# Kernel tuning notes

Measured on AMD Instinct MI355X. Metric: run time of the kernel, lower is better.

## Reference

```python
import jax, jax.numpy as jnp
import numpy as np

NUM_USERS = 100000
NUM_ITEMS = 50000
N_NODES = NUM_USERS + NUM_ITEMS
EMB = 64
N_EDGES = 2000000
NUM_LAYERS = 3


def setup_inputs() -> dict:
    key = jax.random.key(0)
    ks = jax.random.split(key, 16)
    inp = {
        "edge_index": jax.random.randint(ks[0], (2, N_EDGES), 0, N_NODES, dtype=jnp.int64 if jax.config.jax_enable_x64 else jnp.int32),
        "user_features": jax.random.normal(ks[1], (NUM_USERS, 15), dtype=jnp.float32),
        "user_color_indices": jax.random.randint(ks[2], (NUM_USERS,), 0, 22),
        "user_size_indices": jax.random.randint(ks[3], (NUM_USERS,), 0, 18),
        "item_features": jax.random.normal(ks[4], (NUM_ITEMS, 17), dtype=jnp.float32),
        "user_emb_w": jax.random.normal(ks[5], (NUM_USERS, EMB), dtype=jnp.float32) * 0.01,
        "item_emb_w": jax.random.normal(ks[6], (NUM_ITEMS, EMB), dtype=jnp.float32) * 0.01,
        "user_numeric_W": jax.random.normal(ks[7], (EMB, 12), dtype=jnp.float32) * 0.1,
        "user_numeric_b": jnp.zeros((EMB,), dtype=jnp.float32),
        "user_vector_W": jax.random.normal(ks[8], (EMB, 3), dtype=jnp.float32) * 0.1,
        "user_vector_b": jnp.zeros((EMB,), dtype=jnp.float32),
        "color_emb_w": jax.random.normal(ks[9], (22, EMB), dtype=jnp.float32) * 0.1,
        "size_emb_w": jax.random.normal(ks[10], (18, EMB), dtype=jnp.float32) * 0.1,
        "item_numeric_W": jax.random.normal(ks[11], (EMB, 5), dtype=jnp.float32) * 0.1,
        "item_numeric_b": jnp.zeros((EMB,), dtype=jnp.float32),
        "item_vector_W": jax.random.normal(ks[12], (EMB, 12), dtype=jnp.float32) * 0.1,
        "item_vector_b": jnp.zeros((EMB,), dtype=jnp.float32),
    }
    return inp


def _lightgcn_conv(x, row, col, norm):
    # gather x at source (row), scale by per-edge norm, scatter-add at target (col)
    msg = norm[:, None] * x[row]                      # [E, d]
    return jax.ops.segment_sum(msg, col, num_segments=N_NODES)


def reference(edge_index, user_features, user_color_indices, user_size_indices,
              item_features, user_emb_w, item_emb_w,
              user_numeric_W, user_numeric_b, user_vector_W, user_vector_b,
              color_emb_w, size_emb_w,
              item_numeric_W, item_numeric_b, item_vector_W, item_vector_b):
    # multimodal feature fusion
    user_emb = (user_emb_w
                + user_features[:, :12] @ user_numeric_W.T + user_numeric_b
                + user_features[:, 12:15] @ user_vector_W.T + user_vector_b
                + color_emb_w[user_color_indices]
                + size_emb_w[user_size_indices])
    item_emb = (item_emb_w
                + item_features[:, :5] @ item_numeric_W.T + item_numeric_b
                + item_features[:, 5:] @ item_vector_W.T + item_vector_b)
    x = jnp.concatenate([user_emb, item_emb], axis=0)  # [N, d]

    row, col = edge_index[0], edge_index[1]
    # symmetric-normalization coefficients (degree over targets, as in source)
    deg = jax.ops.segment_sum(jnp.ones_like(col, dtype=x.dtype), col, num_segments=N_NODES)
    deg_inv_sqrt = jnp.where(deg > 0, jax.lax.rsqrt(jnp.maximum(deg, 1.0)), 0.0)
    norm = deg_inv_sqrt[row] * deg_inv_sqrt[col]       # [E]

    acc = x
    total = x
    for _ in range(NUM_LAYERS):
        acc = _lightgcn_conv(acc, row, col, norm)      # dropout in eval mode = identity
        total = total + acc
    final = total / (NUM_LAYERS + 1)

    return final[:NUM_USERS], final[NUM_USERS:]
```

## Files before the change

### kernel.cpp

```cpp
#include <hip/hip_runtime.h>

#define EMB 64
#define NBMAX 512
#define BCAP 8192
#define BSTRIDE 12288
#define CHUNK 4096


__device__ __forceinline__ unsigned short f2bf(float f) {
    union { float f; unsigned u; } c; c.f = f;
    unsigned r = c.u + 0x7fffu + ((c.u >> 16) & 1u);
    return (unsigned short)(r >> 16);
}
__device__ __forceinline__ float bflo(unsigned u) {
    union { unsigned u; float f; } c; c.u = u << 16; return c.f;
}
__device__ __forceinline__ float bfhi(unsigned u) {
    union { unsigned u; float f; } c; c.u = u & 0xffff0000u; return c.f;
}
__device__ __forceinline__ unsigned pack2(float a, float b) {
    return (unsigned)f2bf(a) | ((unsigned)f2bf(b) << 16);
}


__global__ void init_kernel(unsigned* __restrict__ p, int nz,
                            unsigned* __restrict__ dummyA,
                            unsigned* __restrict__ dummyB) {
    int i = blockIdx.x * blockDim.x + threadIdx.x;
    if (i < nz) p[i] = 0u;
    if (blockIdx.x == 0) {
        int t = threadIdx.x;
        if (t < 32) dummyA[t] = 0u;
        else if (t < 64) dummyB[t - 32] = 0u;
    }
}


__global__ void fuse_users_kernel(const float* __restrict__ feat,
                                  const int* __restrict__ cidx,
                                  const int* __restrict__ sidx,
                                  const float* __restrict__ emb_w,
                                  const float* __restrict__ Wn,
                                  const float* __restrict__ bn,
                                  const float* __restrict__ Wv,
                                  const float* __restrict__ bv,
                                  const float* __restrict__ color_w,
                                  const float* __restrict__ size_w,
                                  const float* __restrict__ dis,
                                  unsigned short* __restrict__ totB,
                                  unsigned short* __restrict__ y0,
                                  int U) {
    int t = blockIdx.x * blockDim.x + threadIdx.x;
    int u = t >> 6, d = t & 63;
    if (u >= U) return;
    const float* f = feat + (size_t)u * 15;
    float acc = emb_w[(size_t)u * EMB + d] + bn[d] + bv[d];
#pragma unroll
    for (int k = 0; k < 12; ++k) acc = fmaf(f[k], Wn[d * 12 + k], acc);
#pragma unroll
    for (int k = 0; k < 3; ++k) acc = fmaf(f[12 + k], Wv[d * 3 + k], acc);
    acc += color_w[(size_t)cidx[u] * EMB + d];
    acc += size_w[(size_t)sidx[u] * EMB + d];
    size_t o = (size_t)u * EMB + d;
    totB[o] = f2bf(acc);
    y0[o] = f2bf(acc * dis[u]);
}

__global__ void fuse_items_kernel(const float* __restrict__ feat,
                                  const float* __restrict__ emb_w,
                                  const float* __restrict__ Wn,
                                  const float* __restrict__ bn,
                                  const float* __restrict__ Wv,
                                  const float* __restrict__ bv,
                                  const float* __restrict__ dis,
                                  unsigned short* __restrict__ totB,
                                  unsigned short* __restrict__ y0,
                                  int I, int U) {
    int t = blockIdx.x * blockDim.x + threadIdx.x;
    int i = t >> 6, d = t & 63;
    if (i >= I) return;
    const float* f = feat + (size_t)i * 17;
    float acc = emb_w[(size_t)i * EMB + d] + bn[d] + bv[d];
#pragma unroll
    for (int k = 0; k < 5; ++k) acc = fmaf(f[k], Wn[d * 5 + k], acc);
#pragma unroll
    for (int k = 0; k < 12; ++k) acc = fmaf(f[5 + k], Wv[d * 12 + k], acc);
    int n = U + i;
    size_t o = (size_t)n * EMB + d;
    totB[o] = f2bf(acc);
    y0[o] = f2bf(acc * dis[n]);
}


__global__ __launch_bounds__(512) void partition_kernel(
        const int* __restrict__ row, const int* __restrict__ col,
        unsigned* __restrict__ bcursor, unsigned* __restrict__ bucketbuf,
        int E, int NB) {
    __shared__ unsigned h[NBMAX];
    __shared__ unsigned wbase[NBMAX];
    const int t = threadIdx.x;
    const long chunk = (long)blockIdx.x * CHUNK;

    for (int i = t; i < NB; i += 512) h[i] = 0u;
    __syncthreads();
    for (int it = 0; it < CHUNK / 2048; ++it) {
        long e = chunk + (long)it * 2048 + t * 4;
        if (e + 3 < E) {
            uint4 c4 = *reinterpret_cast<const uint4*>(&col[e]);
            atomicAdd(&h[c4.x >> 9], 1u); atomicAdd(&h[c4.y >> 9], 1u);
            atomicAdd(&h[c4.z >> 9], 1u); atomicAdd(&h[c4.w >> 9], 1u);
        } else {
            for (int k = 0; k < 4; ++k) {
                long ek = e + k;
                if (ek < E) atomicAdd(&h[((unsigned)col[ek]) >> 9], 1u);
            }
        }
    }
    __syncthreads();
    for (int i = t; i < NB; i += 512) {
        unsigned c = h[i];
        wbase[i] = c ? atomicAdd(&bcursor[i], c) : 0u;
    }
    __syncthreads();
    for (int i = t; i < NB; i += 512) h[i] = 0u;
    __syncthreads();
    for (int it = 0; it < CHUNK / 2048; ++it) {
        long e = chunk + (long)it * 2048 + t * 4;
        if (e + 3 < E) {
            uint4 c4 = *reinterpret_cast<const uint4*>(&col[e]);
            uint4 r4 = *reinterpret_cast<const uint4*>(&row[e]);
            unsigned cs[4] = {c4.x, c4.y, c4.z, c4.w};
            unsigned rs[4] = {r4.x, r4.y, r4.z, r4.w};
#pragma unroll
            for (int k = 0; k < 4; ++k) {
                unsigned b = cs[k] >> 9;
                unsigned pos = wbase[b] + atomicAdd(&h[b], 1u);
                if (pos < BCAP)
                    bucketbuf[(size_t)b * BCAP + pos] = (rs[k] << 9) | (cs[k] & 511u);
            }
        } else {
            for (int k = 0; k < 4; ++k) {
                long ek = e + k;
                if (ek < E) {
                    unsigned c = (unsigned)col[ek];
                    unsigned b = c >> 9;
                    unsigned pos = wbase[b] + atomicAdd(&h[b], 1u);
                    if (pos < BCAP)
                        bucketbuf[(size_t)b * BCAP + pos] =
                            (((unsigned)row[ek]) << 9) | (c & 511u);
                }
            }
        }
    }
}


__global__ __launch_bounds__(512) void bucket_csr_kernel(
        const unsigned* __restrict__ bcursor,
        const unsigned* __restrict__ bucketbuf,
        uint4* __restrict__ meta,
        float* __restrict__ dis, unsigned* __restrict__ srcidx,
        unsigned* __restrict__ order,
        int N, int NB) {
    const int b = blockIdx.x;
    const int t = threadIdx.x;
    __shared__ unsigned hist[512];
    __shared__ unsigned ps[512];
    __shared__ unsigned cls[64];
    __shared__ unsigned clsB[64];

    const unsigned base = (unsigned)b * BSTRIDE;
    unsigned cntb = bcursor[b];
    if (cntb > BCAP) cntb = BCAP;

    hist[t] = 0u;
    if (t < 64) cls[t] = 0u;
    __syncthreads();
    const unsigned* buf = bucketbuf + (size_t)b * BCAP;
    for (unsigned j = t; j < cntb; j += 512) atomicAdd(&hist[buf[j] & 511u], 1u);
    __syncthreads();

    unsigned h0 = hist[t];
    unsigned c0p = (h0 + 7u) & ~7u;
    ps[t] = c0p;
    __syncthreads();
    for (int off = 1; off < 512; off <<= 1) {
        unsigned y = (t >= off) ? ps[t - off] : 0u;
        __syncthreads();
        ps[t] += y;
        __syncthreads();
    }
    unsigned beg0 = base + ps[t] - c0p;

    int n0 = (b << 9) + t;
    unsigned c = min(c0p >> 3, 63u), lpos = 0;
    if (n0 < N) {
        float dv = h0 ? rsqrtf((float)h0) : 0.f;
        meta[n0] = make_uint4(beg0, beg0 + c0p, __float_as_uint(dv), 0u);
        dis[n0] = dv;
        lpos = atomicAdd(&cls[c], 1u);
        for (unsigned k = h0; k < c0p; ++k) srcidx[beg0 + k] = ((unsigned)N) << 5;
    }
    __syncthreads();
    if (t == 0) {
        unsigned run = 0;
        for (int i = 0; i < 64; ++i) { unsigned v = cls[i]; clsB[i] = run; run += v; }
    }
    __syncthreads();
    if (n0 < N) order[(b << 9) + clsB[c] + lpos] = (unsigned)n0;

    hist[t] = beg0;
    __syncthreads();
    for (unsigned j = t; j < cntb; j += 512) {
        unsigned p = buf[j];
        unsigned pos = atomicAdd(&hist[p & 511u], 1u);
        srcidx[pos] = (p >> 9) << 5;
    }
}


__global__ __launch_bounds__(256) void gather_propagate_kernel(
        const unsigned* __restrict__ order, const uint4* __restrict__ meta,
        const unsigned* __restrict__ src,
        const unsigned* __restrict__ srcidx,
        unsigned* __restrict__ ynext,
        unsigned* __restrict__ totB,
        float4* __restrict__ outF,
        int N, int mode) {
    int lane = threadIdx.x & 63;
    int slot = blockIdx.x * 8 + ((threadIdx.x >> 6) << 1) + (lane >> 5);
    bool active = slot < N;
    int n = active ? (int)order[slot] : 0;
    uint4 md = active ? meta[n] : make_uint4(0u, 0u, 0u, 0u);
    unsigned beg = md.x, endp = md.y;
    float dn = __uint_as_float(md.z);
    unsigned q = (unsigned)((lane >> 4) & 1);
    unsigned m2 = (unsigned)(lane & 15) * 2u;
    size_t o = (size_t)n * 32 + m2;
    uint2 tv = *reinterpret_cast<const uint2*>(&totB[o]);
    float s0 = 0.f, s1 = 0.f, s2 = 0.f, s3 = 0.f;
    float t0 = 0.f, t1 = 0.f, t2 = 0.f, t3 = 0.f;
    unsigned j = beg;
    for (; j + 16 <= endp; j += 16) {
        uint4 iv0 = *reinterpret_cast<const uint4*>(&srcidx[j + 4u * q]);
        uint4 iv1 = *reinterpret_cast<const uint4*>(&srcidx[j + 8u + 4u * q]);
        uint2 ua = *reinterpret_cast<const uint2*>(&src[iv0.x + m2]);
        uint2 ub = *reinterpret_cast<const uint2*>(&src[iv0.y + m2]);
        uint2 uc = *reinterpret_cast<const uint2*>(&src[iv0.z + m2]);
        uint2 ud = *reinterpret_cast<const uint2*>(&src[iv0.w + m2]);
        uint2 ue = *reinterpret_cast<const uint2*>(&src[iv1.x + m2]);
        uint2 uf = *reinterpret_cast<const uint2*>(&src[iv1.y + m2]);
        uint2 ug = *reinterpret_cast<const uint2*>(&src[iv1.z + m2]);
        uint2 uh = *reinterpret_cast<const uint2*>(&src[iv1.w + m2]);
        s0 += (bflo(ua.x) + bflo(ub.x)) + (bflo(uc.x) + bflo(ud.x));
        s1 += (bfhi(ua.x) + bfhi(ub.x)) + (bfhi(uc.x) + bfhi(ud.x));
        s2 += (bflo(ua.y) + bflo(ub.y)) + (bflo(uc.y) + bflo(ud.y));
        s3 += (bfhi(ua.y) + bfhi(ub.y)) + (bfhi(uc.y) + bfhi(ud.y));
        t0 += (bflo(ue.x) + bflo(uf.x)) + (bflo(ug.x) + bflo(uh.x));
        t1 += (bfhi(ue.x) + bfhi(uf.x)) + (bfhi(ug.x) + bfhi(uh.x));
        t2 += (bflo(ue.y) + bflo(uf.y)) + (bflo(ug.y) + bflo(uh.y));
        t3 += (bfhi(ue.y) + bfhi(uf.y)) + (bfhi(ug.y) + bfhi(uh.y));
    }
    if (j < endp) {
        uint4 iv = *reinterpret_cast<const uint4*>(&srcidx[j + 4u * q]);
        uint2 ua = *reinterpret_cast<const uint2*>(&src[iv.x + m2]);
        uint2 ub = *reinterpret_cast<const uint2*>(&src[iv.y + m2]);
        uint2 uc = *reinterpret_cast<const uint2*>(&src[iv.z + m2]);
        uint2 ud = *reinterpret_cast<const uint2*>(&src[iv.w + m2]);
        s0 += (bflo(ua.x) + bflo(ub.x)) + (bflo(uc.x) + bflo(ud.x));
        s1 += (bfhi(ua.x) + bfhi(ub.x)) + (bfhi(uc.x) + bfhi(ud.x));
        s2 += (bflo(ua.y) + bflo(ub.y)) + (bflo(uc.y) + bflo(ud.y));
        s3 += (bfhi(ua.y) + bfhi(ub.y)) + (bfhi(uc.y) + bfhi(ud.y));
    }
    s0 += t0; s1 += t1; s2 += t2; s3 += t3;
    s0 += __shfl_xor(s0, 16);
    s1 += __shfl_xor(s1, 16);
    s2 += __shfl_xor(s2, 16);
    s3 += __shfl_xor(s3, 16);
    if (active && (lane & 31) < 16) {
        float a0 = dn * s0, a1 = dn * s1, a2 = dn * s2, a3 = dn * s3;
        float b0 = bflo(tv.x) + a0, b1 = bfhi(tv.x) + a1;
        float b2 = bflo(tv.y) + a2, b3 = bfhi(tv.y) + a3;
        if (mode == 0) {
            uint2 nv;
            nv.x = pack2(b0, b1);
            nv.y = pack2(b2, b3);
            *reinterpret_cast<uint2*>(&totB[o]) = nv;
            uint2 pk;
            pk.x = pack2(dn * a0, dn * a1);
            pk.y = pack2(dn * a2, dn * a3);
            *reinterpret_cast<uint2*>(&ynext[(size_t)n * 32 + m2]) = pk;
        } else {
            outF[(size_t)n * 16 + (m2 >> 1)] =
                make_float4(b0 * 0.25f, b1 * 0.25f, b2 * 0.25f, b3 * 0.25f);
        }
    }
}


extern "C" void kernel_launch(void* const* d_in, const int* in_sizes, int n_in,
                              void* d_out, int out_size, void* d_ws, size_t ws_size,
                              hipStream_t stream) {
    const int*   edge       = (const int*)d_in[0];
    const float* user_feat  = (const float*)d_in[1];
    const int*   cidx       = (const int*)d_in[2];
    const int*   sidx       = (const int*)d_in[3];
    const float* item_feat  = (const float*)d_in[4];
    const float* user_emb_w = (const float*)d_in[5];
    const float* item_emb_w = (const float*)d_in[6];
    const float* uWn        = (const float*)d_in[7];
    const float* ubn        = (const float*)d_in[8];
    const float* uWv        = (const float*)d_in[9];
    const float* ubv        = (const float*)d_in[10];
    const float* color_w    = (const float*)d_in[11];
    const float* size_w     = (const float*)d_in[12];
    const float* iWn        = (const float*)d_in[13];
    const float* ibn        = (const float*)d_in[14];
    const float* iWv        = (const float*)d_in[15];
    const float* ibv        = (const float*)d_in[16];

    const int E = in_sizes[0] / 2;
    const int U = in_sizes[5] / EMB;
    const int I = in_sizes[6] / EMB;
    const int N = U + I;
    const int NB = (N + 511) >> 9;

    const int* row = edge;
    const int* col = edge + E;

    unsigned short* yA      = (unsigned short*)d_ws;
    unsigned short* yB      = yA + (size_t)(N + 1) * EMB;
    unsigned*       bucketbuf = (unsigned*)yB;
    unsigned short* totB    = yB + (size_t)(N + 1) * EMB;
    unsigned*       srcidx  = (unsigned*)(totB + (size_t)N * EMB);
    uint4*          meta    = (uint4*)(srcidx + (size_t)NB * BSTRIDE);
    float*          dis     = (float*)(meta + N);
    unsigned*       bcursor = (unsigned*)(dis + N);
    unsigned*       order   = bcursor + NB;

    const int TB = 256;

    init_kernel<<<(NB + TB - 1) / TB, TB, 0, stream>>>(
        bcursor, NB,
        (unsigned*)(yA + (size_t)N * EMB), (unsigned*)(yB + (size_t)N * EMB));
    const int gP = (E + CHUNK - 1) / CHUNK;
    partition_kernel<<<gP, 512, 0, stream>>>(row, col, bcursor, bucketbuf, E, NB);
    bucket_csr_kernel<<<NB, 512, 0, stream>>>(bcursor, bucketbuf, meta, dis,
                                              srcidx, order, N, NB);

    {
        int gU = (int)(((long)U * EMB + TB - 1) / TB);
        fuse_users_kernel<<<gU, TB, 0, stream>>>(user_feat, cidx, sidx, user_emb_w,
                                                 uWn, ubn, uWv, ubv, color_w, size_w,
                                                 dis, totB, yA, U);
        int gI = (int)(((long)I * EMB + TB - 1) / TB);
        fuse_items_kernel<<<gI, TB, 0, stream>>>(item_feat, item_emb_w,
                                                 iWn, ibn, iWv, ibv,
                                                 dis, totB, yA, I, U);
    }

    const int gG = (N + 7) / 8;
    gather_propagate_kernel<<<gG, TB, 0, stream>>>(order, meta,
                                                   (const unsigned*)yA, srcidx,
                                                   (unsigned*)yB, (unsigned*)totB,
                                                   (float4*)d_out, N, 0);
    gather_propagate_kernel<<<gG, TB, 0, stream>>>(order, meta,
                                                   (const unsigned*)yB, srcidx,
                                                   (unsigned*)yA, (unsigned*)totB,
                                                   (float4*)d_out, N, 0);
    gather_propagate_kernel<<<gG, TB, 0, stream>>>(order, meta,
                                                   (const unsigned*)yA, srcidx,
                                                   (unsigned*)yB, (unsigned*)totB,
                                                   (float4*)d_out, N, 1);

    (void)n_in; (void)out_size; (void)ws_size;
}
```

Measured before the change: 236.6 us.

## Merge fuse kernels, cache partition/bucket values in registers, reverse degree class order

Folds the separate user and item fusion kernels into one launch. Each thread now computes two embedding dims and writes packed bf16 pairs. The partition kernel keeps the col values from its histogram pass in registers so they are not reloaded, and the bucket CSR kernel keeps its bucket entries in registers for the second scatter pass. The degree class ordering is reversed so that high-degree nodes are scheduled first in the gather. The trade-off is higher register pressure, and the unrolled 16-entry register array assumes each bucket holds at most 8192 entries.

```diff
diff --git a/kernel.cpp b/kernel.cpp
--- a/kernel.cpp
+++ b/kernel.cpp
@@ -36,59 +36,71 @@
 }
 
 
-__global__ void fuse_users_kernel(const float* __restrict__ feat,
-                                  const int* __restrict__ cidx,
-                                  const int* __restrict__ sidx,
-                                  const float* __restrict__ emb_w,
-                                  const float* __restrict__ Wn,
-                                  const float* __restrict__ bn,
-                                  const float* __restrict__ Wv,
-                                  const float* __restrict__ bv,
-                                  const float* __restrict__ color_w,
-                                  const float* __restrict__ size_w,
-                                  const float* __restrict__ dis,
-                                  unsigned short* __restrict__ totB,
-                                  unsigned short* __restrict__ y0,
-                                  int U) {
+__global__ __launch_bounds__(256) void fuse_kernel(
+        const float* __restrict__ ufeat,
+        const int* __restrict__ cidx, const int* __restrict__ sidx,
+        const float* __restrict__ uemb,
+        const float* __restrict__ uWn, const float* __restrict__ ubn,
+        const float* __restrict__ uWv, const float* __restrict__ ubv,
+        const float* __restrict__ color_w,
+        const float* __restrict__ size_w,
+        const float* __restrict__ ifeat,
+        const float* __restrict__ iemb,
+        const float* __restrict__ iWn, const float* __restrict__ ibn,
+        const float* __restrict__ iWv, const float* __restrict__ ibv,
+        const float* __restrict__ dis,
+        unsigned* __restrict__ totB,
+        unsigned* __restrict__ y0,
+        int U, int N) {
     int t = blockIdx.x * blockDim.x + threadIdx.x;
-    int u = t >> 6, d = t & 63;
-    if (u >= U) return;
-    const float* f = feat + (size_t)u * 15;
-    float acc = emb_w[(size_t)u * EMB + d] + bn[d] + bv[d];
-#pragma unroll
-    for (int k = 0; k < 12; ++k) acc = fmaf(f[k], Wn[d * 12 + k], acc);
-#pragma unroll
-    for (int k = 0; k < 3; ++k) acc = fmaf(f[12 + k], Wv[d * 3 + k], acc);
-    acc += color_w[(size_t)cidx[u] * EMB + d];
-    acc += size_w[(size_t)sidx[u] * EMB + d];
-    size_t o = (size_t)u * EMB + d;
-    totB[o] = f2bf(acc);
-    y0[o] = f2bf(acc * dis[u]);
-}
-
-__global__ void fuse_items_kernel(const float* __restrict__ feat,
-                                  const float* __restrict__ emb_w,
-                                  const float* __restrict__ Wn,
-                                  const float* __restrict__ bn,
-                                  const float* __restrict__ Wv,
-                                  const float* __restrict__ bv,
-                                  const float* __restrict__ dis,
-                                  unsigned short* __restrict__ totB,
-                                  unsigned short* __restrict__ y0,
-                                  int I, int U) {
-    int t = blockIdx.x * blockDim.x + threadIdx.x;
-    int i = t >> 6, d = t & 63;
-    if (i >= I) return;
-    const float* f = feat + (size_t)i * 17;
-    float acc = emb_w[(size_t)i * EMB + d] + bn[d] + bv[d];
-#pragma unroll
-    for (int k = 0; k < 5; ++k) acc = fmaf(f[k], Wn[d * 5 + k], acc);
-#pragma unroll
-    for (int k = 0; k < 12; ++k) acc = fmaf(f[5 + k], Wv[d * 12 + k], acc);
-    int n = U + i;
-    size_t o = (size_t)n * EMB + d;
-    totB[o] = f2bf(acc);
-    y0[o] = f2bf(acc * dis[n]);
+    int n = t >> 5, m = t & 31;
+    if (n >= N) return;
+    int d0 = m * 2, d1 = d0 + 1;
+    float acc0, acc1;
+    if (n < U) {
+        const float* f = ufeat + (size_t)n * 15;
+        float2 e = *reinterpret_cast<const float2*>(&uemb[(size_t)n * EMB + d0]);
+        acc0 = e.x + ubn[d0] + ubv[d0];
+        acc1 = e.y + ubn[d1] + ubv[d1];
+#pragma unroll
+        for (int k = 0; k < 12; ++k) {
+            float fv = f[k];
+            acc0 = fmaf(fv, uWn[d0 * 12 + k], acc0);
+            acc1 = fmaf(fv, uWn[d1 * 12 + k], acc1);
+        }
+#pragma unroll
+        for (int k = 0; k < 3; ++k) {
+            float fv = f[12 + k];
+            acc0 = fmaf(fv, uWv[d0 * 3 + k], acc0);
+            acc1 = fmaf(fv, uWv[d1 * 3 + k], acc1);
+        }
+        float2 cw = *reinterpret_cast<const float2*>(&color_w[(size_t)cidx[n] * EMB + d0]);
+        float2 sw = *reinterpret_cast<const float2*>(&size_w[(size_t)sidx[n] * EMB + d0]);
+        acc0 += cw.x + sw.x;
+        acc1 += cw.y + sw.y;
+    } else {
+        int i = n - U;
+        const float* f = ifeat + (size_t)i * 17;
+        float2 e = *reinterpret_cast<const float2*>(&iemb[(size_t)i * EMB + d0]);
+        acc0 = e.x + ibn[d0] + ibv[d0];
+        acc1 = e.y + ibn[d1] + ibv[d1];
+#pragma unroll
+        for (int k = 0; k < 5; ++k) {
+            float fv = f[k];
+            acc0 = fmaf(fv, iWn[d0 * 5 + k], acc0);
+            acc1 = fmaf(fv, iWn[d1 * 5 + k], acc1);
+        }
+#pragma unroll
+        for (int k = 0; k < 12; ++k) {
+            float fv = f[5 + k];
+            acc0 = fmaf(fv, iWv[d0 * 12 + k], acc0);
+            acc1 = fmaf(fv, iWv[d1 * 12 + k], acc1);
+        }
+    }
+    float dv = dis[n];
+    size_t o = (size_t)n * 32 + m;
+    totB[o] = pack2(acc0, acc1);
+    y0[o] = pack2(acc0 * dv, acc1 * dv);
 }
 
 
@@ -103,16 +115,22 @@
 
     for (int i = t; i < NB; i += 512) h[i] = 0u;
     __syncthreads();
-    for (int it = 0; it < CHUNK / 2048; ++it) {
-        long e = chunk + (long)it * 2048 + t * 4;
-        if (e + 3 < E) {
+    unsigned cc[2][4];
+#pragma unroll
+    for (int it = 0; it < 2; ++it) {
+        long e = chunk + (long)it * 2048 + (long)t * 4;
+        if (e + 3 < (long)E) {
             uint4 c4 = *reinterpret_cast<const uint4*>(&col[e]);
+            cc[it][0] = c4.x; cc[it][1] = c4.y; cc[it][2] = c4.z; cc[it][3] = c4.w;
             atomicAdd(&h[c4.x >> 9], 1u); atomicAdd(&h[c4.y >> 9], 1u);
             atomicAdd(&h[c4.z >> 9], 1u); atomicAdd(&h[c4.w >> 9], 1u);
         } else {
+#pragma unroll
             for (int k = 0; k < 4; ++k) {
                 long ek = e + k;
-                if (ek < E) atomicAdd(&h[((unsigned)col[ek]) >> 9], 1u);
+                unsigned cv = (ek < (long)E) ? (unsigned)col[ek] : 0xffffffffu;
+                cc[it][k] = cv;
+                if (cv != 0xffffffffu) atomicAdd(&h[cv >> 9], 1u);
             }
         }
     }
@@ -124,30 +142,31 @@
     __syncthreads();
     for (int i = t; i < NB; i += 512) h[i] = 0u;
     __syncthreads();
-    for (int it = 0; it < CHUNK / 2048; ++it) {
-        long e = chunk + (long)it * 2048 + t * 4;
-        if (e + 3 < E) {
-            uint4 c4 = *reinterpret_cast<const uint4*>(&col[e]);
+#pragma unroll
+    for (int it = 0; it < 2; ++it) {
+        long e = chunk + (long)it * 2048 + (long)t * 4;
+        if (e + 3 < (long)E) {
             uint4 r4 = *reinterpret_cast<const uint4*>(&row[e]);
-            unsigned cs[4] = {c4.x, c4.y, c4.z, c4.w};
             unsigned rs[4] = {r4.x, r4.y, r4.z, r4.w};
 #pragma unroll
             for (int k = 0; k < 4; ++k) {
-                unsigned b = cs[k] >> 9;
+                unsigned cv = cc[it][k];
+                unsigned b = cv >> 9;
                 unsigned pos = wbase[b] + atomicAdd(&h[b], 1u);
                 if (pos < BCAP)
-                    bucketbuf[(size_t)b * BCAP + pos] = (rs[k] << 9) | (cs[k] & 511u);
+                    bucketbuf[(size_t)b * BCAP + pos] = (rs[k] << 9) | (cv & 511u);
             }
         } else {
+#pragma unroll
             for (int k = 0; k < 4; ++k) {
                 long ek = e + k;
-                if (ek < E) {
-                    unsigned c = (unsigned)col[ek];
-                    unsigned b = c >> 9;
+                unsigned cv = cc[it][k];
+                if (cv != 0xffffffffu) {
+                    unsigned b = cv >> 9;
                     unsigned pos = wbase[b] + atomicAdd(&h[b], 1u);
                     if (pos < BCAP)
                         bucketbuf[(size_t)b * BCAP + pos] =
-                            (((unsigned)row[ek]) << 9) | (c & 511u);
+                            (((unsigned)row[ek]) << 9) | (cv & 511u);
                 }
             }
         }
@@ -177,7 +196,14 @@
     if (t < 64) cls[t] = 0u;
     __syncthreads();
     const unsigned* buf = bucketbuf + (size_t)b * BCAP;
-    for (unsigned j = t; j < cntb; j += 512) atomicAdd(&hist[buf[j] & 511u], 1u);
+    unsigned rv[16];
+#pragma unroll
+    for (int it = 0; it < 16; ++it) {
+        unsigned j = (unsigned)t + (unsigned)it * 512u;
+        unsigned p = (j < cntb) ? buf[j] : 0xffffffffu;
+        rv[it] = p;
+        if (p != 0xffffffffu) atomicAdd(&hist[p & 511u], 1u);
+    }
     __syncthreads();
 
     unsigned h0 = hist[t];
@@ -193,7 +219,8 @@
     unsigned beg0 = base + ps[t] - c0p;
 
     int n0 = (b << 9) + t;
-    unsigned c = min(c0p >> 3, 63u), lpos = 0;
+    unsigned c = 63u - min(c0p >> 3, 63u);
+    unsigned lpos = 0;
     if (n0 < N) {
         float dv = h0 ? rsqrtf((float)h0) : 0.f;
         meta[n0] = make_uint4(beg0, beg0 + c0p, __float_as_uint(dv), 0u);
@@ -211,10 +238,13 @@
 
     hist[t] = beg0;
     __syncthreads();
-    for (unsigned j = t; j < cntb; j += 512) {
-        unsigned p = buf[j];
-        unsigned pos = atomicAdd(&hist[p & 511u], 1u);
-        srcidx[pos] = (p >> 9) << 5;
+#pragma unroll
+    for (int it = 0; it < 16; ++it) {
+        unsigned p = rv[it];
+        if (p != 0xffffffffu) {
+            unsigned pos = atomicAdd(&hist[p & 511u], 1u);
+            srcidx[pos] = (p >> 9) << 5;
+        }
     }
 }
 
@@ -349,14 +379,11 @@
                                               srcidx, order, N, NB);
 
     {
-        int gU = (int)(((long)U * EMB + TB - 1) / TB);
-        fuse_users_kernel<<<gU, TB, 0, stream>>>(user_feat, cidx, sidx, user_emb_w,
-                                                 uWn, ubn, uWv, ubv, color_w, size_w,
-                                                 dis, totB, yA, U);
-        int gI = (int)(((long)I * EMB + TB - 1) / TB);
-        fuse_items_kernel<<<gI, TB, 0, stream>>>(item_feat, item_emb_w,
-                                                 iWn, ibn, iWv, ibv,
-                                                 dis, totB, yA, I, U);
+        long tF = (long)N * 32;
+        fuse_kernel<<<(int)((tF + TB - 1) / TB), TB, 0, stream>>>(
+            user_feat, cidx, sidx, user_emb_w, uWn, ubn, uWv, ubv,
+            color_w, size_w, item_feat, item_emb_w, iWn, ibn, iWv, ibv,
+            dis, (unsigned*)totB, (unsigned*)yA, U, N);
     }
 
     const int gG = (N + 7) / 8;
```

After: 231.0 us. 1.02x faster.
